# Optimization experiments

Hardware: AMD Instinct MI355X
Metric: run time of the kernel (lower is better)

## Reference

```python
import jax, jax.numpy as jnp
import numpy as np


def setup_inputs() -> dict:
    key = jax.random.key(0)
    k1, k2, k3 = jax.random.split(key, 3)
    B, D, H = 16384, 256, 64
    X = jax.random.normal(k1, (B, D), dtype=jnp.float32)
    AUX = jax.random.normal(k2, (B, (1 + D) * H), dtype=jnp.float32)
    K = jax.random.randint(k3, (B,), 0, 129, dtype=jnp.int64)  # idx in [0, M=128]
    return {"X": X, "AUX": AUX, "K": K}


def reference(X, AUX, K):
    B, D = X.shape
    H = AUX.shape[1] // (1 + D)
    M = D // 2
    # Per-sample weight matrix W[b] of shape (1+D, H)
    W = AUX.reshape(B, 1 + D, H)
    # Original zeros rows idx:M and M+idx: (end), i.e. keeps row j iff
    #   j < idx  OR  (M <= j < M + idx)
    j = jnp.arange(1 + D)  # row indices 0..D (row D is the bias row)
    Kc = K[:, None]
    keep = (j < Kc) | ((j >= M) & (j < M + Kc))  # [B, 1+D] bool
    # Y[b] = concat(X[b], 1.0); apply mask to Y instead of W (same dot product)
    Y = jnp.concatenate([X, jnp.ones((B, 1), dtype=X.dtype)], axis=1)
    Ym = Y * keep.astype(X.dtype)
    dot = jnp.einsum("bj,bjh->bh", Ym, W)  # [B, H]
    return jnp.tanh(dot)
```

## Files before the change

### kernel.cpp

```cpp
#include <hip/hip_runtime.h>
#include <cmath>


#define D_DIM 256
#define H_DIM 64
#define ROWS 257
#define ROWSTRIDE (ROWS * H_DIM)

__global__ __launch_bounds__(256, 8)
void dotmask_kernel(const float* __restrict__ X,
                    const float* __restrict__ AUX,
                    const int* __restrict__ K,
                    float* __restrict__ out)
{
    const int b    = blockIdx.x;
    const int tid  = threadIdx.x;
    const int lane = tid & 63;
    const int w    = tid >> 6;
    const int jo   = lane >> 4;
    const int h4   = (lane & 15) * 4;

    const int k = K[b];
    const float* __restrict__ Wb  = AUX + (size_t)b * ROWSTRIDE;
    const float* __restrict__ WbH = Wb + h4;
    const float* __restrict__ Xb  = X   + (size_t)b * D_DIM;

    float ax = 0.f, ay = 0.f, az = 0.f, aw = 0.f;

    for (int j0 = w * 4; j0 < k; j0 += 32) {
        const int ja   = j0 + jo;
        const int ja2  = (ja + 128 > 256) ? 256 : (ja + 128);
        const float4 wa1 = *reinterpret_cast<const float4*>(WbH + ((size_t)ja  << 6));
        const float4 wa2 = *reinterpret_cast<const float4*>(WbH + ((size_t)ja2 << 6));
        const float  xa1r = Xb[ja];
        const float  xa2r = Xb[(ja + 128 > 255) ? 255 : (ja + 128)];

        const int j0b = j0 + 16;
        const bool doB = (j0b < k);
        float4 wb1 = make_float4(0,0,0,0), wb2 = make_float4(0,0,0,0);
        float  xb1r = 0.f, xb2r = 0.f;
        int jb = 0;
        if (doB) {
            jb = j0b + jo;
            const int jb2 = (jb + 128 > 256) ? 256 : (jb + 128);
            wb1 = *reinterpret_cast<const float4*>(WbH + ((size_t)jb  << 6));
            wb2 = *reinterpret_cast<const float4*>(WbH + ((size_t)jb2 << 6));
            xb1r = Xb[jb];
            xb2r = Xb[(jb + 128 > 255) ? 255 : (jb + 128)];
        }

        const float xa1 = (ja < k) ? xa1r : 0.f;
        const float xa2 = (ja < k) ? xa2r : 0.f;
        ax += xa1 * wa1.x; ay += xa1 * wa1.y; az += xa1 * wa1.z; aw += xa1 * wa1.w;
        ax += xa2 * wa2.x; ay += xa2 * wa2.y; az += xa2 * wa2.z; aw += xa2 * wa2.w;

        const float xb1 = (doB && jb < k) ? xb1r : 0.f;
        const float xb2 = (doB && jb < k) ? xb2r : 0.f;
        ax += xb1 * wb1.x; ay += xb1 * wb1.y; az += xb1 * wb1.z; aw += xb1 * wb1.w;
        ax += xb2 * wb2.x; ay += xb2 * wb2.y; az += xb2 * wb2.z; aw += xb2 * wb2.w;
    }

    if (k > 128 && w == 0 && jo == 0) {
        const float4 wv = *reinterpret_cast<const float4*>(Wb + (size_t)256 * H_DIM + h4);
        ax += wv.x; ay += wv.y; az += wv.z; aw += wv.w;
    }

    ax += __shfl_xor(ax, 16); ay += __shfl_xor(ay, 16);
    az += __shfl_xor(az, 16); aw += __shfl_xor(aw, 16);
    ax += __shfl_xor(ax, 32); ay += __shfl_xor(ay, 32);
    az += __shfl_xor(az, 32); aw += __shfl_xor(aw, 32);

    __shared__ float lds[4][H_DIM];
    if (lane < 16) {
        float4 p; p.x = ax; p.y = ay; p.z = az; p.w = aw;
        *reinterpret_cast<float4*>(&lds[w][h4]) = p;
    }
    __syncthreads();

    if (tid < H_DIM) {
        const float s = lds[0][tid] + lds[1][tid] + lds[2][tid] + lds[3][tid];
        out[(size_t)b * H_DIM + tid] = tanhf(s);
    }
}

extern "C" void kernel_launch(void* const* d_in, const int* in_sizes, int n_in,
                              void* d_out, int out_size, void* d_ws, size_t ws_size,
                              hipStream_t stream)
{
    const float* X   = (const float*)d_in[0];
    const float* AUX = (const float*)d_in[1];
    const int*   K   = (const int*)d_in[2];
    float* out = (float*)d_out;

    const int B = in_sizes[2];
    dotmask_kernel<<<B, 256, 0, stream>>>(X, AUX, K, out);
}
```

Baseline: 114.2 us.

## Schedule blocks in descending K order via counting sort for load balance

Adds count, scan and scatter kernels that bucket samples by K and build a permutation listing samples from largest to smallest K. The main kernel then maps blockIdx through that permutation, so heavy blocks are dispatched first and light ones fill the tail. This targets load imbalance from variable per-sample work, at the cost of three extra launches, a memset, and atomics on a few hot counters.

Result: slower. 146.2 us (+28.1%).

```diff
diff --git a/kernel.cpp b/kernel.cpp
--- a/kernel.cpp
+++ b/kernel.cpp
@@ -7,13 +7,46 @@
 #define ROWS 257
 #define ROWSTRIDE (ROWS * H_DIM)
 
+#define WS_COUNTS 0
+#define WS_CURSOR 129
+#define WS_ORDER  512
+
+__global__ void count_kernel(const int* __restrict__ K, int* __restrict__ counts, int B)
+{
+    const int i = blockIdx.x * 256 + threadIdx.x;
+    if (i < B) atomicAdd(&counts[K[i]], 1);
+}
+
+__global__ void scan_kernel(int* __restrict__ counts, int* __restrict__ cursor)
+{
+    if (threadIdx.x == 0) {
+        int off = 0;
+        for (int k = 128; k >= 0; --k) {
+            const int c = counts[k];
+            cursor[k] = off;
+            off += c;
+        }
+    }
+}
+
+__global__ void scatter_kernel(const int* __restrict__ K, int* __restrict__ cursor,
+                               int* __restrict__ order, int B)
+{
+    const int i = blockIdx.x * 256 + threadIdx.x;
+    if (i < B) {
+        const int p = atomicAdd(&cursor[K[i]], 1);
+        order[p] = i;
+    }
+}
+
 __global__ __launch_bounds__(256, 8)
 void dotmask_kernel(const float* __restrict__ X,
                     const float* __restrict__ AUX,
                     const int* __restrict__ K,
+                    const int* __restrict__ order,
                     float* __restrict__ out)
 {
-    const int b    = blockIdx.x;
+    const int b    = order[blockIdx.x];
     const int tid  = threadIdx.x;
     const int lane = tid & 63;
     const int w    = tid >> 6;
@@ -91,7 +124,16 @@
     const float* AUX = (const float*)d_in[1];
     const int*   K   = (const int*)d_in[2];
     float* out = (float*)d_out;
+    int*   wsi = (int*)d_ws;
 
     const int B = in_sizes[2];
-    dotmask_kernel<<<B, 256, 0, stream>>>(X, AUX, K, out);
+    const int nb = (B + 255) / 256;
+
+    hipMemsetAsync(wsi + WS_COUNTS, 0, 129 * sizeof(int), stream);
+
+    count_kernel  <<<nb, 256, 0, stream>>>(K, wsi + WS_COUNTS, B);
+    scan_kernel   <<<1, 64, 0, stream>>>(wsi + WS_COUNTS, wsi + WS_CURSOR);
+    scatter_kernel<<<nb, 256, 0, stream>>>(K, wsi + WS_CURSOR, wsi + WS_ORDER, B);
+
+    dotmask_kernel<<<B, 256, 0, stream>>>(X, AUX, K, wsi + WS_ORDER, out);
 }
```
